# Kernel tuning notes

Hardware: AMD Instinct MI355X
Metric: run time of the kernel (lower is better)

## Reference

```python
import jax, jax.numpy as jnp
import numpy as np

FS = 48000          # sample_rate
C = 343.0           # sound speed
MAX_ORDER = 10
T = 24000           # RIR buffer length
W = 81              # fractional-delay sinc filter length
HALF = W // 2
BETA = 0.9          # wall reflection coefficient
OFFSET = 40.0       # global delay offset (matches shoebox_origin = 40 + fs*d/c)
NEG_SLOPE = 0.01    # torch LeakyReLU default


def _mlp(x, W1, b1, W2, b2, W3, b3):
    h = jax.nn.leaky_relu(x @ W1.T + b1, NEG_SLOPE)
    h = jax.nn.leaky_relu(h @ W2.T + b2, NEG_SLOPE)
    return jax.nn.sigmoid(h @ W3.T + b3)  # [B, 9]


def _image_source_rir(room, mic, src):
    """Batched shoebox image-source RIR synthesis with windowed-sinc scatter.

    room, mic, src: [B, 3]. Returns rir: [B, T].
    """
    B = room.shape[0]
    k = jnp.arange(-MAX_ORDER, MAX_ORDER + 1)          # [K], K = 21
    even = (k % 2 == 0)

    def axis_images(a):
        L = room[:, a:a + 1]                           # [B, 1]
        s = src[:, a:a + 1]                            # [B, 1]
        # even k: k*L + s ; odd k: (k+1)*L - s  (standard 1-D mirror images)
        return jnp.where(even[None, :], k[None, :] * L + s,
                         (k[None, :] + 1) * L - s)     # [B, K]

    ix, iy, iz = axis_images(0), axis_images(1), axis_images(2)
    dx = ix[:, :, None, None] - mic[:, 0, None, None, None]
    dy = iy[:, None, :, None] - mic[:, 1, None, None, None]
    dz = iz[:, None, None, :] - mic[:, 2, None, None, None]
    d = jnp.sqrt(dx * dx + dy * dy + dz * dz)          # [B, K, K, K]

    ka = jnp.abs(k)
    order = (ka[:, None, None] + ka[None, :, None] + ka[None, None, :])  # [K,K,K]

    d = d.reshape(B, -1)                               # [B, K^3]
    order_f = order.reshape(-1).astype(d.dtype)        # [K^3]
    valid_order = order.reshape(-1) <= MAX_ORDER

    amp = jnp.where(valid_order[None, :],
                    (BETA ** order_f)[None, :] / (4.0 * jnp.pi * jnp.maximum(d, 1e-3)),
                    0.0)                               # [B, K^3]

    delay = OFFSET + FS * d / C                        # fractional sample delay
    t0 = jnp.floor(delay)
    frac = delay - t0                                  # grad flows through delay
    t0 = t0.astype(jnp.int32)

    j = jnp.arange(W)
    hann = 0.5 * (1.0 - jnp.cos(2.0 * jnp.pi * j / (W - 1)))
    # windowed fractional-delay sinc taps: [B, K^3, W]
    taps = jnp.sinc((j - HALF)[None, None, :].astype(d.dtype) - frac[..., None]) * hann
    vals = amp[..., None] * taps                       # [B, K^3, W]

    idx = t0[..., None] + (j - HALF)                   # [B, K^3, W]
    in_range = (idx >= 0) & (idx < T)
    vals = jnp.where(in_range, vals, 0.0)
    idx = jnp.clip(idx, 0, T - 1)

    b = jnp.arange(B)[:, None, None]
    return jnp.zeros((B, T), vals.dtype).at[b, idx].add(vals)


def setup_inputs() -> dict:
    key = jax.random.key(0)
    ks = jax.random.split(key, 7)
    B = 128
    inp = {
        "input": jax.random.normal(ks[0], (B, 22), dtype=jnp.float32),
        "W1": jax.random.normal(ks[1], (30, 22), dtype=jnp.float32) * 0.2,
        "b1": jax.random.normal(ks[2], (30,), dtype=jnp.float32) * 0.05,
        "W2": jax.random.normal(ks[3], (20, 30), dtype=jnp.float32) * 0.2,
        "b2": jax.random.normal(ks[4], (20,), dtype=jnp.float32) * 0.05,
        "W3": jax.random.normal(ks[5], (9, 20), dtype=jnp.float32) * 0.2,
        "b3": jax.random.normal(ks[6], (9,), dtype=jnp.float32) * 0.05,
    }
    return inp


def reference(input, W1, b1, W2, b2, W3, b3):
    z = _mlp(input, W1, b1, W2, b2, W3, b3)            # [B, 9] in (0,1)
    room = z[:, 0:3] * 20.0                            # room dims in (0, 20) m
    mic = z[:, 3:6] * room                             # mic inside room
    src = z[:, 6:9] * room                             # source inside room
    rir = _image_source_rir(room, mic, src)            # [B, 24000]
    dist = jnp.linalg.norm(mic - src, axis=1)          # [B]
    origin = 40.0 + FS * dist / C                      # [B]
    return rir, origin
```

## Files before the change

kernel.cpp:

```cpp
#include <hip/hip_runtime.h>
#include <math.h>

#define T_LEN      24000
#define W_LEN      81
#define HALF_W     40
#define NK         21
#define MAXORD     10
#define NIMG_TOTAL 1561
#define NROUNDS    25
#define NB         376
#define GSAMP      128
#define NGRP       188
#define FS_F       48000.0f
#define C_F        343.0f
#define FS_OVER_C  (48000.0f / 343.0f)
#define PI_F       3.14159265358979323846f
#define HSTEP      (2.0f * PI_F / 80.0f)
#define INV_4PI_F  0.07957747154594767f
#define LOG2_BETA  (-0.15200309344504997f)
#define NEG_SLOPE  0.01f

#define HDR_I      384
#define ROW_BYTES  (HDR_I * 4 + 1600 * 16)

struct Table { unsigned int e[NROUNDS * 64]; };
constexpr Table make_table() {
    Table t{};
    int n = 0;
    for (int kx = 0; kx < NK; ++kx)
        for (int ky = 0; ky < NK; ++ky)
            for (int kz = 0; kz < NK; ++kz) {
                int ax = kx >= MAXORD ? kx - MAXORD : MAXORD - kx;
                int ay = ky >= MAXORD ? ky - MAXORD : MAXORD - ky;
                int az = kz >= MAXORD ? kz - MAXORD : MAXORD - kz;
                int order = ax + ay + az;
                if (order <= MAXORD)
                    t.e[n++] = (unsigned)((order << 15) | (kx << 10) | (ky << 5) | kz);
            }
    for (int i = n; i < NROUNDS * 64; ++i) t.e[i] = t.e[n - 1];
    return t;
}
__constant__ Table g_tbl = make_table();

__global__ __launch_bounds__(256)
void rir_prep_kernel(const float* __restrict__ g_in,
                     const float* __restrict__ W1, const float* __restrict__ b1,
                     const float* __restrict__ W2, const float* __restrict__ b2,
                     const float* __restrict__ W3, const float* __restrict__ b3,
                     unsigned char* __restrict__ ws, float* __restrict__ out_origin)
{
    __shared__ float dsq[3 * NK];
    __shared__ float h1[30], h2[20], zb[9], sm_in[22], rms[9];
    __shared__ int counts[NB], offs[NB + 1], cursor[NB];

    const int tid  = threadIdx.x;
    const int lane = tid & 63;
    const int w    = tid >> 6;
    const int b    = blockIdx.x;

    for (int i = tid; i < NB; i += 256) { counts[i] = 0; cursor[i] = 0; }

    if (w == 0) {
        if (lane < 22) sm_in[lane] = g_in[b * 22 + lane];
        if (lane < 30) {
            float a = b1[lane];
            const float* wp = W1 + lane * 22;
            #pragma unroll
            for (int i = 0; i < 22; ++i) a += sm_in[i] * wp[i];
            h1[lane] = (a >= 0.0f) ? a : NEG_SLOPE * a;
        }
        if (lane < 20) {
            float a = b2[lane];
            const float* wp = W2 + lane * 30;
            #pragma unroll
            for (int i = 0; i < 30; ++i) a += h1[i] * wp[i];
            h2[lane] = (a >= 0.0f) ? a : NEG_SLOPE * a;
        }
        if (lane < 9) {
            float a = b3[lane];
            const float* wp = W3 + lane * 20;
            #pragma unroll
            for (int i = 0; i < 20; ++i) a += h2[i] * wp[i];
            zb[lane] = 1.0f / (1.0f + __expf(-a));
        }
        if (lane < 3) {
            float room = zb[lane] * 20.0f;
            rms[lane]     = room;
            rms[3 + lane] = zb[3 + lane] * room;
            rms[6 + lane] = zb[6 + lane] * room;
        }
        if (lane == 0) {
            float dx = rms[3] - rms[6], dy = rms[4] - rms[7], dz = rms[5] - rms[8];
            out_origin[b] = 40.0f + FS_F * sqrtf(dx * dx + dy * dy + dz * dz) / C_F;
        }
        if (lane < 3 * NK) {
            int a  = lane / NK;
            int kk = (lane - a * NK) - MAXORD;
            float L = rms[a], src = rms[6 + a];
            float img = ((kk & 1) == 0) ? (float)kk * L + src : (float)(kk + 1) * L - src;
            float diff = img - rms[3 + a];
            dsq[lane] = diff * diff;
        }
    }
    __syncthreads();

    for (int r = w; r < NROUNDS; r += 4) {
        int gi = r * 64 + lane;
        unsigned e = g_tbl.e[gi];
        int kzi = e & 31, kyi = (e >> 5) & 31, kxi = (e >> 10) & 31;
        float d   = sqrtf(dsq[kxi] + dsq[NK + kyi] + dsq[2 * NK + kzi]);
        float dly = 40.0f + d * FS_OVER_C;
        int   t0  = (int)floorf(dly);
        bool live = (gi < NIMG_TOTAL) && (t0 - HALF_W < T_LEN);
        if (live) atomicAdd(&counts[t0 >> 6], 1);
    }
    __syncthreads();

    if (w == 0) {
        const int base = lane * 6;
        int c[6], s0 = 0;
        #pragma unroll
        for (int j = 0; j < 6; ++j) {
            int idx = base + j;
            c[j] = (idx < NB) ? counts[idx] : 0;
            s0 += c[j];
        }
        int incl = s0;
        #pragma unroll
        for (int off = 1; off < 64; off <<= 1) {
            int t = __shfl_up(incl, off);
            if (lane >= off) incl += t;
        }
        int acc = incl - s0;
        #pragma unroll
        for (int j = 0; j < 6; ++j) {
            int idx = base + j;
            if (idx < NB) offs[idx] = acc;
            acc += c[j];
        }
        if (lane == 63) offs[NB] = acc;
    }
    __syncthreads();

    unsigned char* rowp = ws + (size_t)b * ROW_BYTES;
    int*    hdr  = (int*)rowp;
    float4* prow = (float4*)(rowp + HDR_I * 4);

    for (int r = w; r < NROUNDS; r += 4) {
        int gi = r * 64 + lane;
        unsigned e = g_tbl.e[gi];
        int kzi = e & 31, kyi = (e >> 5) & 31, kxi = (e >> 10) & 31, order = (int)(e >> 15);
        float d   = sqrtf(dsq[kxi] + dsq[NK + kyi] + dsq[2 * NK + kzi]);
        float dly = 40.0f + d * FS_OVER_C;
        float t0f = floorf(dly);
        int   t0  = (int)t0f;
        bool live = (gi < NIMG_TOTAL) && (t0 - HALF_W < T_LEN);
        if (live) {
            float frac = dly - t0f;
            float amp  = exp2f((float)order * LOG2_BETA) * INV_4PI_F
                         * __builtin_amdgcn_rcpf(fmaxf(d, 0.001f));
            float sp   = __sinf(PI_F * frac);
            int rank = offs[t0 >> 6] + atomicAdd(&cursor[t0 >> 6], 1);
            prow[rank] = make_float4(amp * sp, frac, amp, t0f);
        }
    }
    __syncthreads();

    for (int i = tid; i <= NB; i += 256) hdr[i] = offs[i];
}

__global__ __launch_bounds__(256)
void rir_gather4_kernel(const unsigned char* __restrict__ ws,
                        float* __restrict__ out_rir)
{
    __shared__ float buf[GSAMP];
    __shared__ float hann[W_LEN + 7];

    const int tid  = threadIdx.x;
    const int lane = tid & 63;
    const int w    = tid >> 6;
    const int grp  = blockIdx.x;
    const int b    = blockIdx.y;
    const int g0   = grp * GSAMP;

    const unsigned char* rowp = ws + (size_t)b * ROW_BYTES;
    const int*    hdr  = (const int*)rowp;
    const float4* prow = (const float4*)(rowp + HDR_I * 4);

    const int blo   = max(g0 - HALF_W, 0) >> 6;
    const int bhi   = min(g0 + GSAMP - 1 + HALF_W, T_LEN + HALF_W - 1) >> 6;
    const int start = hdr[blo];
    const int end   = hdr[bhi + 1];

    if (tid < GSAMP) buf[tid] = 0.0f;
    if (tid >= 128 && tid < 128 + W_LEN)
        hann[tid - 128] = 0.5f - 0.5f * __cosf((float)(tid - 128) * HSTEP);
    __syncthreads();

    float acc0 = 0.0f, acc1 = 0.0f;
    const float gf0 = (float)(g0 + lane);

    #pragma unroll 2
    for (int i = start + w; i < end; i += 4) {
        float4 p = prow[i];
        float n0 = gf0 - p.w;
        float n1 = n0 + 64.0f;

        if (fabsf(n0) <= 40.0f) {
            float x  = n0 - p.y;
            int   ni = (int)n0;
            float sg = (ni & 1) ? p.x : -p.x;
            float v  = (x == 0.0f) ? p.z : sg * __builtin_amdgcn_rcpf(PI_F * x);
            acc0 += v * hann[ni + HALF_W];
        }
        if (fabsf(n1) <= 40.0f) {
            float x  = n1 - p.y;
            int   ni = (int)n1;
            float sg = (ni & 1) ? p.x : -p.x;
            float v  = (x == 0.0f) ? p.z : sg * __builtin_amdgcn_rcpf(PI_F * x);
            acc1 += v * hann[ni + HALF_W];
        }
    }

    if (acc0 != 0.0f) atomicAdd(&buf[lane], acc0);
    if (acc1 != 0.0f) atomicAdd(&buf[lane + 64], acc1);
    __syncthreads();

    const int g = g0 + tid;
    if (tid < GSAMP && g < T_LEN)
        out_rir[(size_t)b * T_LEN + g] = buf[tid];
}

#define FTS 448
#define FNSLICE 54
__global__ __launch_bounds__(64)
void rir_wave_kernel(const float* __restrict__ g_in,
                     const float* __restrict__ W1, const float* __restrict__ b1,
                     const float* __restrict__ W2, const float* __restrict__ b2,
                     const float* __restrict__ W3, const float* __restrict__ b3,
                     float* __restrict__ out_rir, float* __restrict__ out_origin)
{
    __shared__ __align__(16) float rirw[FTS];
    __shared__ float dsq[3 * NK];
    __shared__ float h1[30], h2[20], zb[9], sm_in[22], rms[9];

    const int lane = threadIdx.x;
    const int s    = blockIdx.x;
    const int b    = blockIdx.y;
    const int lo   = s * FTS;
    const int nout = min(FTS, T_LEN - lo);

    float4* rir4 = (float4*)rirw;
    rir4[lane] = make_float4(0.f, 0.f, 0.f, 0.f);
    if (lane < FTS / 4 - 64) rir4[64 + lane] = make_float4(0.f, 0.f, 0.f, 0.f);

    const float c1p = PI_F * (float)(lane - HALF_W);
    const float hw1 = 0.5f - 0.5f * __cosf((float)lane * HSTEP);
    const float hw2 = 0.5f - 0.5f * __cosf((float)(lane + 64) * HSTEP);
    const float sg  = (lane & 1) ? 1.0f : -1.0f;

    if (lane < 22) sm_in[lane] = g_in[b * 22 + lane];
    if (lane < 30) {
        float a = b1[lane];
        const float* wp = W1 + lane * 22;
        #pragma unroll
        for (int i = 0; i < 22; ++i) a += sm_in[i] * wp[i];
        h1[lane] = (a >= 0.0f) ? a : NEG_SLOPE * a;
    }
    if (lane < 20) {
        float a = b2[lane];
        const float* wp = W2 + lane * 30;
        #pragma unroll
        for (int i = 0; i < 30; ++i) a += h1[i] * wp[i];
        h2[lane] = (a >= 0.0f) ? a : NEG_SLOPE * a;
    }
    if (lane < 9) {
        float a = b3[lane];
        const float* wp = W3 + lane * 20;
        #pragma unroll
        for (int i = 0; i < 20; ++i) a += h2[i] * wp[i];
        zb[lane] = 1.0f / (1.0f + __expf(-a));
    }
    if (lane < 3) {
        float room = zb[lane] * 20.0f;
        rms[lane]     = room;
        rms[3 + lane] = zb[3 + lane] * room;
        rms[6 + lane] = zb[6 + lane] * room;
    }
    if (lane == 0 && s == 0) {
        float dx = rms[3] - rms[6], dy = rms[4] - rms[7], dz = rms[5] - rms[8];
        out_origin[b] = 40.0f + FS_F * sqrtf(dx * dx + dy * dy + dz * dz) / C_F;
    }
    if (lane < 3 * NK) {
        int a  = lane / NK;
        int kk = (lane - a * NK) - MAXORD;
        float L = rms[a], src = rms[6 + a];
        float img = ((kk & 1) == 0) ? (float)kk * L + src : (float)(kk + 1) * L - src;
        float diff = img - rms[3 + a];
        dsq[lane] = diff * diff;
    }

    const float lof = (float)(lo - HALF_W);
    const float hif = (float)(lo + nout - 1 + HALF_W);

    for (int r = 0; r < NROUNDS; ++r) {
        unsigned e = g_tbl.e[r * 64 + lane];
        bool live  = (r * 64 + lane) < NIMG_TOTAL;
        int kzi = e & 31, kyi = (e >> 5) & 31, kxi = (e >> 10) & 31, order = (int)(e >> 15);
        float d    = sqrtf(dsq[kxi] + dsq[NK + kyi] + dsq[2 * NK + kzi]);
        float dlyv = 40.0f + d * FS_OVER_C;
        float t0f  = floorf(dlyv);
        float ampv = exp2f((float)order * LOG2_BETA) * INV_4PI_F
                     * __builtin_amdgcn_rcpf(fmaxf(d, 0.001f));
        bool hit = live && (t0f >= lof) && (t0f <= hif);

        unsigned long long mask = __ballot(hit);
        while (mask) {
            int l0 = __builtin_ctzll(mask); mask &= mask - 1;
            float a0 = __shfl(ampv, l0), d0 = __shfl(dlyv, l0);
            float t0b  = floorf(d0);
            float frac = d0 - t0b;
            float sp   = __sinf(PI_F * frac);
            float pv   = sg * sp;
            int   idx  = (int)t0b - HALF_W + lane - lo;
            float x1p  = c1p - PI_F * frac;
            float sv1  = (x1p == 0.0f) ? 1.0f : pv * __builtin_amdgcn_rcpf(x1p);
            if ((unsigned)idx < (unsigned)nout)
                atomicAdd(&rirw[idx], a0 * sv1 * hw1);
            if (lane < 17) {
                int idx2 = idx + 64;
                float sv2 = pv * __builtin_amdgcn_rcpf(x1p + 64.0f * PI_F);
                if ((unsigned)idx2 < (unsigned)nout)
                    atomicAdd(&rirw[idx2], a0 * sv2 * hw2);
            }
        }
    }

    const int n4 = nout / 4;
    float4* out4 = (float4*)(out_rir + (size_t)b * T_LEN + lo);
    out4[lane] = rir4[lane];
    if (lane + 64 < n4) out4[lane + 64] = rir4[lane + 64];
}

extern "C" void kernel_launch(void* const* d_in, const int* in_sizes, int n_in,
                              void* d_out, int out_size, void* d_ws, size_t ws_size,
                              hipStream_t stream) {
    const float* g_in = (const float*)d_in[0];
    const float* W1   = (const float*)d_in[1];
    const float* b1   = (const float*)d_in[2];
    const float* W2   = (const float*)d_in[3];
    const float* b2   = (const float*)d_in[4];
    const float* W3   = (const float*)d_in[5];
    const float* b3   = (const float*)d_in[6];

    const int B = in_sizes[0] / 22;

    float* out_rir    = (float*)d_out;
    float* out_origin = out_rir + (size_t)B * T_LEN;

    const size_t need_ws = (size_t)B * ROW_BYTES;

    if (ws_size >= need_ws) {
        unsigned char* ws = (unsigned char*)d_ws;
        rir_prep_kernel<<<B, 256, 0, stream>>>(
            g_in, W1, b1, W2, b2, W3, b3, ws, out_origin);
        dim3 grid2(NGRP, B);
        rir_gather4_kernel<<<grid2, 256, 0, stream>>>(ws, out_rir);
    } else {
        dim3 grid(FNSLICE, B);
        rir_wave_kernel<<<grid, 64, 0, stream>>>(
            g_in, W1, b1, W2, b2, W3, b3, out_rir, out_origin);
    }
}
```

Before: 62.89 us.

## Widen gather tiles to 256 samples and cache delays in prep kernel

The gather kernel now covers 256 output samples per block, with each lane accumulating four samples. Each loaded pulse record is reused across more outputs, and the number of blocks and overlapping header/window reads is halved. The prep kernel runs 512 threads and stores each image's delay in shared memory during the counting pass, so the scatter pass skips recomputing distances. It also precomputes the beta^order amplitude table and recovers distance from the delay. Larger tiles mean fewer blocks in flight and more wasted window checks per pulse, and recovering distance from the delay may introduce small rounding differences.

New measurement: 63.13 us. Within noise of the previous version (+0.4%).

```diff
diff --git a/kernel.cpp b/kernel.cpp
--- a/kernel.cpp
+++ b/kernel.cpp
@@ -9,11 +9,12 @@
 #define NIMG_TOTAL 1561
 #define NROUNDS    25
 #define NB         376
-#define GSAMP      128
-#define NGRP       188
+#define GSAMP      256
+#define NGRP       94
 #define FS_F       48000.0f
 #define C_F        343.0f
 #define FS_OVER_C  (48000.0f / 343.0f)
+#define C_OVER_FS  (343.0f / 48000.0f)
 #define PI_F       3.14159265358979323846f
 #define HSTEP      (2.0f * PI_F / 80.0f)
 #define INV_4PI_F  0.07957747154594767f
@@ -42,7 +43,7 @@
 }
 __constant__ Table g_tbl = make_table();
 
-__global__ __launch_bounds__(256)
+__global__ __launch_bounds__(512)
 void rir_prep_kernel(const float* __restrict__ g_in,
                      const float* __restrict__ W1, const float* __restrict__ b1,
                      const float* __restrict__ W2, const float* __restrict__ b2,
@@ -51,6 +52,8 @@
 {
     __shared__ float dsq[3 * NK];
     __shared__ float h1[30], h2[20], zb[9], sm_in[22], rms[9];
+    __shared__ float bp[MAXORD + 1];
+    __shared__ float dlys[NROUNDS * 64];
     __shared__ int counts[NB], offs[NB + 1], cursor[NB];
 
     const int tid  = threadIdx.x;
@@ -58,8 +61,10 @@
     const int w    = tid >> 6;
     const int b    = blockIdx.x;
 
-    for (int i = tid; i < NB; i += 256) { counts[i] = 0; cursor[i] = 0; }
-
+    for (int i = tid; i < NB; i += 512) { counts[i] = 0; cursor[i] = 0; }
+
+    if (w == 1 && lane <= MAXORD)
+        bp[lane] = exp2f((float)lane * LOG2_BETA) * INV_4PI_F;
     if (w == 0) {
         if (lane < 22) sm_in[lane] = g_in[b * 22 + lane];
         if (lane < 30) {
@@ -104,7 +109,7 @@
     }
     __syncthreads();
 
-    for (int r = w; r < NROUNDS; r += 4) {
+    for (int r = w; r < NROUNDS; r += 8) {
         int gi = r * 64 + lane;
         unsigned e = g_tbl.e[gi];
         int kzi = e & 31, kyi = (e >> 5) & 31, kxi = (e >> 10) & 31;
@@ -112,6 +117,7 @@
         float dly = 40.0f + d * FS_OVER_C;
         int   t0  = (int)floorf(dly);
         bool live = (gi < NIMG_TOTAL) && (t0 - HALF_W < T_LEN);
+        dlys[gi] = live ? dly : 1.0e9f;
         if (live) atomicAdd(&counts[t0 >> 6], 1);
     }
     __syncthreads();
@@ -146,32 +152,29 @@
     int*    hdr  = (int*)rowp;
     float4* prow = (float4*)(rowp + HDR_I * 4);
 
-    for (int r = w; r < NROUNDS; r += 4) {
+    for (int r = w; r < NROUNDS; r += 8) {
         int gi = r * 64 + lane;
-        unsigned e = g_tbl.e[gi];
-        int kzi = e & 31, kyi = (e >> 5) & 31, kxi = (e >> 10) & 31, order = (int)(e >> 15);
-        float d   = sqrtf(dsq[kxi] + dsq[NK + kyi] + dsq[2 * NK + kzi]);
-        float dly = 40.0f + d * FS_OVER_C;
-        float t0f = floorf(dly);
-        int   t0  = (int)t0f;
-        bool live = (gi < NIMG_TOTAL) && (t0 - HALF_W < T_LEN);
-        if (live) {
+        float dly = dlys[gi];
+        if (dly < 1.0e8f) {
+            int order = (int)(g_tbl.e[gi] >> 15);
+            float t0f  = floorf(dly);
             float frac = dly - t0f;
-            float amp  = exp2f((float)order * LOG2_BETA) * INV_4PI_F
-                         * __builtin_amdgcn_rcpf(fmaxf(d, 0.001f));
+            float d    = (dly - 40.0f) * C_OVER_FS;
+            float amp  = bp[order] * __builtin_amdgcn_rcpf(fmaxf(d, 0.001f));
             float sp   = __sinf(PI_F * frac);
-            int rank = offs[t0 >> 6] + atomicAdd(&cursor[t0 >> 6], 1);
+            int bin  = (int)t0f;
+            int rank = offs[bin >> 6] + atomicAdd(&cursor[bin >> 6], 1);
             prow[rank] = make_float4(amp * sp, frac, amp, t0f);
         }
     }
     __syncthreads();
 
-    for (int i = tid; i <= NB; i += 256) hdr[i] = offs[i];
+    for (int i = tid; i <= NB; i += 512) hdr[i] = offs[i];
 }
 
 __global__ __launch_bounds__(256)
-void rir_gather4_kernel(const unsigned char* __restrict__ ws,
-                        float* __restrict__ out_rir)
+void rir_gather256_kernel(const unsigned char* __restrict__ ws,
+                          float* __restrict__ out_rir)
 {
     __shared__ float buf[GSAMP];
     __shared__ float hann[W_LEN + 7];
@@ -192,42 +195,38 @@
     const int start = hdr[blo];
     const int end   = hdr[bhi + 1];
 
-    if (tid < GSAMP) buf[tid] = 0.0f;
+    buf[tid] = 0.0f;
     if (tid >= 128 && tid < 128 + W_LEN)
         hann[tid - 128] = 0.5f - 0.5f * __cosf((float)(tid - 128) * HSTEP);
     __syncthreads();
 
-    float acc0 = 0.0f, acc1 = 0.0f;
+    float acc[4] = {0.f, 0.f, 0.f, 0.f};
     const float gf0 = (float)(g0 + lane);
 
     #pragma unroll 2
     for (int i = start + w; i < end; i += 4) {
         float4 p = prow[i];
         float n0 = gf0 - p.w;
-        float n1 = n0 + 64.0f;
-
-        if (fabsf(n0) <= 40.0f) {
-            float x  = n0 - p.y;
-            int   ni = (int)n0;
-            float sg = (ni & 1) ? p.x : -p.x;
-            float v  = (x == 0.0f) ? p.z : sg * __builtin_amdgcn_rcpf(PI_F * x);
-            acc0 += v * hann[ni + HALF_W];
-        }
-        if (fabsf(n1) <= 40.0f) {
-            float x  = n1 - p.y;
-            int   ni = (int)n1;
-            float sg = (ni & 1) ? p.x : -p.x;
-            float v  = (x == 0.0f) ? p.z : sg * __builtin_amdgcn_rcpf(PI_F * x);
-            acc1 += v * hann[ni + HALF_W];
-        }
-    }
-
-    if (acc0 != 0.0f) atomicAdd(&buf[lane], acc0);
-    if (acc1 != 0.0f) atomicAdd(&buf[lane + 64], acc1);
+        #pragma unroll
+        for (int k = 0; k < 4; ++k) {
+            float n = n0 + 64.0f * (float)k;
+            if (fabsf(n) <= 40.0f) {
+                float x  = n - p.y;
+                int   ni = (int)n;
+                float sg = (ni & 1) ? p.x : -p.x;
+                float v  = (x == 0.0f) ? p.z : sg * __builtin_amdgcn_rcpf(PI_F * x);
+                acc[k] += v * hann[ni + HALF_W];
+            }
+        }
+    }
+
+    #pragma unroll
+    for (int k = 0; k < 4; ++k)
+        if (acc[k] != 0.0f) atomicAdd(&buf[lane + 64 * k], acc[k]);
     __syncthreads();
 
     const int g = g0 + tid;
-    if (tid < GSAMP && g < T_LEN)
+    if (g < T_LEN)
         out_rir[(size_t)b * T_LEN + g] = buf[tid];
 }
 
@@ -362,10 +361,10 @@
 
     if (ws_size >= need_ws) {
         unsigned char* ws = (unsigned char*)d_ws;
-        rir_prep_kernel<<<B, 256, 0, stream>>>(
+        rir_prep_kernel<<<B, 512, 0, stream>>>(
             g_in, W1, b1, W2, b2, W3, b3, ws, out_origin);
         dim3 grid2(NGRP, B);
-        rir_gather4_kernel<<<grid2, 256, 0, stream>>>(ws, out_rir);
+        rir_gather256_kernel<<<grid2, 256, 0, stream>>>(ws, out_rir);
     } else {
         dim3 grid(FNSLICE, B);
         rir_wave_kernel<<<grid, 64, 0, stream>>>(
```
